# Kernel tuning notes

Hardware: AMD Instinct MI355X
Metric: run time of the kernel (lower is better)

Reference implementation:

```python
import jax, jax.numpy as jnp
import numpy as np
import math

D_MODEL = 512
EXPAND = 2
D_INNER = EXPAND * D_MODEL          # 1024
HEADDIM = 16
NHEADS = D_INNER // HEADDIM         # 64
NGROUPS = 1
D_STATE = 16
D_CONV = 4
CHUNK = 256
CONV_DIM = D_INNER + 2 * NGROUPS * D_STATE      # 1056
D_IN_PROJ = 2 * D_INNER + 2 * NGROUPS * D_STATE + NHEADS  # 2144
EPS = 1e-5


def setup_inputs() -> dict:
    key = jax.random.key(0)
    ks = jax.random.split(key, 9)
    B, L = 2, 4096
    u = jax.random.normal(ks[0], (B, L, D_MODEL), dtype=jnp.float32)
    in_proj_w = jax.random.normal(ks[1], (D_IN_PROJ, D_MODEL), dtype=jnp.float32) * (1.0 / math.sqrt(D_MODEL))
    conv_w = jax.random.normal(ks[2], (CONV_DIM, D_CONV), dtype=jnp.float32) * (1.0 / math.sqrt(D_CONV))
    conv_b = jnp.zeros((CONV_DIM,), dtype=jnp.float32)
    # dt_bias = inverse-softplus of dt sampled log-uniform in [1e-3, 1e-1]
    dt = jnp.exp(jax.random.uniform(ks[3], (NHEADS,)) * (math.log(0.1) - math.log(0.001)) + math.log(0.001))
    dt_bias = dt + jnp.log(-jnp.expm1(-dt))
    A_log = jnp.log(jax.random.uniform(ks[4], (NHEADS,), minval=1.0, maxval=16.0))
    D_skip = jnp.ones((NHEADS,), dtype=jnp.float32)
    norm_w = jnp.ones((D_INNER,), dtype=jnp.float32)
    out_proj_w = jax.random.normal(ks[5], (D_MODEL, D_INNER), dtype=jnp.float32) * (1.0 / math.sqrt(D_INNER))
    return {"u": u, "in_proj_w": in_proj_w, "conv_w": conv_w, "conv_b": conv_b,
            "dt_bias": dt_bias, "A_log": A_log, "D_skip": D_skip,
            "norm_w": norm_w, "out_proj_w": out_proj_w}


def _segsum(x):
    # x: (..., T) -> (..., T, T) lower-triangular cumulative segment sums
    T = x.shape[-1]
    cs = jnp.cumsum(x, axis=-1)
    s = cs[..., :, None] - cs[..., None, :]
    mask = jnp.tril(jnp.ones((T, T), dtype=bool))
    return jnp.where(mask, s, -jnp.inf)


def _ssd(xdt, dA, Bm, Cm):
    # xdt: (b,l,h,p) already multiplied by dt; dA: (b,l,h); Bm,Cm: (b,l,h,n)
    b, l, h, p = xdt.shape
    n = Bm.shape[-1]
    nc = l // CHUNK
    xr = xdt.reshape(b, nc, CHUNK, h, p)
    Br = Bm.reshape(b, nc, CHUNK, h, n)
    Cr = Cm.reshape(b, nc, CHUNK, h, n)
    dAr = dA.reshape(b, nc, CHUNK, h).transpose(0, 3, 1, 2)  # (b,h,nc,c)
    A_cs = jnp.cumsum(dAr, axis=-1)
    # intra-chunk (diagonal blocks)
    Ldec = jnp.exp(_segsum(dAr))                              # (b,h,nc,c,c)
    Y_diag = jnp.einsum('bclhn,bcshn,bhcls,bcshp->bclhp', Cr, Br, Ldec, xr)
    # per-chunk final states
    decay_states = jnp.exp(A_cs[..., -1:] - A_cs)             # (b,h,nc,c)
    states = jnp.einsum('bclhn,bhcl,bclhp->bchpn', Br, decay_states, xr)
    states = jnp.concatenate([jnp.zeros_like(states[:, :1]), states], axis=1)
    chunk_sums = jnp.pad(A_cs[..., -1], ((0, 0), (0, 0), (1, 0)))  # (b,h,nc+1)
    decay_chunk = jnp.exp(_segsum(chunk_sums))                # (b,h,nc+1,nc+1)
    new_states = jnp.einsum('bhzc,bchpn->bzhpn', decay_chunk, states)
    prev_states = new_states[:, :-1]                          # (b,nc,h,p,n)
    # inter-chunk contribution
    state_decay_out = jnp.exp(A_cs)                           # (b,h,nc,c)
    Y_off = jnp.einsum('bclhn,bchpn,bhcl->bclhp', Cr, prev_states, state_decay_out)
    return (Y_diag + Y_off).reshape(b, l, h, p)


def _forward(u, in_proj_w, conv_w, conv_b, dt_bias, A_log, D_skip, norm_w, out_proj_w):
    b, l, _ = u.shape
    zxbcdt = jnp.einsum('bld,ed->ble', u, in_proj_w)
    z = zxbcdt[..., :D_INNER]
    xBC = zxbcdt[..., D_INNER:D_INNER + CONV_DIM]
    dt = zxbcdt[..., D_INNER + CONV_DIM:]
    dt = jax.nn.softplus(dt + dt_bias)                        # (b,l,h)
    # causal depthwise conv1d + silu
    xBC_t = xBC.transpose(0, 2, 1)                            # (b, conv_dim, l)
    conv_out = jax.lax.conv_general_dilated(
        xBC_t, conv_w[:, None, :], window_strides=(1,),
        padding=[(D_CONV - 1, 0)], feature_group_count=CONV_DIM,
        dimension_numbers=('NCH', 'OIH', 'NCH'))
    xBC = jax.nn.silu((conv_out + conv_b[None, :, None]).transpose(0, 2, 1))
    x = xBC[..., :D_INNER].reshape(b, l, NHEADS, HEADDIM)
    Bg = xBC[..., D_INNER:D_INNER + NGROUPS * D_STATE].reshape(b, l, NGROUPS, D_STATE)
    Cg = xBC[..., D_INNER + NGROUPS * D_STATE:].reshape(b, l, NGROUPS, D_STATE)
    hpg = NHEADS // NGROUPS
    Bm = jnp.repeat(Bg, hpg, axis=2)                          # (b,l,h,n)
    Cm = jnp.repeat(Cg, hpg, axis=2)
    A = -jnp.exp(A_log)                                       # (h,)
    dA = dt * A                                               # (b,l,h)
    y = _ssd(x * dt[..., None], dA, Bm, Cm)
    y = y + x * D_skip[None, None, :, None]
    y = y.reshape(b, l, D_INNER)
    # gated RMSNorm (norm_before_gate=False): norm(y * silu(z)) * w
    y = y * jax.nn.silu(z)
    y = y * jax.lax.rsqrt(jnp.mean(y * y, axis=-1, keepdims=True) + EPS) * norm_w
    return jnp.einsum('ble,de->bld', y, out_proj_w)


def reference(u, in_proj_w, conv_w, conv_b, dt_bias, A_log, D_skip, norm_w, out_proj_w):
    return _forward(u, in_proj_w, conv_w, conv_b, dt_bias, A_log, D_skip, norm_w, out_proj_w)
```

## Files before the change

### kernel.cpp

```cpp
#include <hip/hip_runtime.h>
#include <hip/hip_bf16.h>
#include <math.h>

#define D_MODEL   512
#define D_INNER   1024
#define NHEADS    64
#define HEADDIM   16
#define D_STATE   16
#define CONV_DIM  1056
#define D_IN_PROJ 2144
#define CHUNK     256
#define NCHUNK    16
#define BATCH     2
#define SEQ       4096
#define ROWS      (BATCH * SEQ)
#define LDZX      2176
#define TPAD      144

typedef __bf16    bf16x8 __attribute__((ext_vector_type(8)));
typedef _Float16  f16x8  __attribute__((ext_vector_type(8)));
typedef float     f32x4  __attribute__((ext_vector_type(4)));
typedef float     f32x16 __attribute__((ext_vector_type(16)));
typedef unsigned short u16x8 __attribute__((ext_vector_type(8)));
typedef unsigned int   u32x4 __attribute__((ext_vector_type(4)));

__device__ __forceinline__ float softplusf(float x) {
    return (x > 20.f) ? x : log1pf(expf(x));
}
__device__ __forceinline__ float siluf(float x) {
    return x / (1.f + expf(-x));
}
__device__ __forceinline__ unsigned short f2b(float x) {
    union { __hip_bfloat16 h; unsigned short u; } cv;
    cv.h = __float2bfloat16(x);
    return cv.u;
}
__device__ __forceinline__ float b2f(unsigned short u) {
    union { float f; unsigned int i; } c;
    c.i = (unsigned int)u << 16;
    return c.f;
}
__device__ __forceinline__ void load_lds16(const unsigned short* g, unsigned short* l) {
    __builtin_amdgcn_global_load_lds(
        (const __attribute__((address_space(1))) void*)g,
        (__attribute__((address_space(3))) void*)l,
        16, 0, 0);
}

__global__ __launch_bounds__(256) void cast8(const float* __restrict__ in,
                                             unsigned short* __restrict__ out, int n) {
    int i = (blockIdx.x * blockDim.x + threadIdx.x) * 8;
    if (i >= n) return;
    float4 a = *(const float4*)(in + i);
    float4 b = *(const float4*)(in + i + 4);
    u16x8 o;
    o[0] = f2b(a.x); o[1] = f2b(a.y); o[2] = f2b(a.z); o[3] = f2b(a.w);
    o[4] = f2b(b.x); o[5] = f2b(b.y); o[6] = f2b(b.z); o[7] = f2b(b.w);
    *(u16x8*)(out + i) = o;
}

__global__ __launch_bounds__(256) void castpad8(const float* __restrict__ in,
                                                unsigned short* __restrict__ out,
                                                int n, int npad) {
    int i = (blockIdx.x * blockDim.x + threadIdx.x) * 8;
    if (i >= npad) return;
    u16x8 o;
    if (i + 8 <= n) {
        float4 a = *(const float4*)(in + i);
        float4 b = *(const float4*)(in + i + 4);
        o[0] = f2b(a.x); o[1] = f2b(a.y); o[2] = f2b(a.z); o[3] = f2b(a.w);
        o[4] = f2b(b.x); o[5] = f2b(b.y); o[6] = f2b(b.z); o[7] = f2b(b.w);
    } else {
        #pragma unroll
        for (int j = 0; j < 8; ++j) o[j] = (i + j < n) ? f2b(in[i + j]) : (unsigned short)0;
    }
    *(u16x8*)(out + i) = o;
}

__global__ __launch_bounds__(256) void gemm_in(const unsigned short* __restrict__ A,
                                               const unsigned short* __restrict__ B,
                                               unsigned short* __restrict__ C16,
                                               float* __restrict__ dtsp,
                                               const float* __restrict__ dtb) {
    __shared__ unsigned short smem[128 * TPAD];
    const int t    = threadIdx.x;
    const int wave = t >> 6;
    const int lane = t & 63;
    const int bid  = blockIdx.x;
    const int swz  = (bid & 7) * 136 + (bid >> 3);
    const int by   = swz / 17;
    const int bx   = swz - by * 17;
    const int bm   = by * 128;
    const int bn   = bx * 128;
    const int wr   = wave >> 1;
    const int wc   = wave & 1;

    const int srow = wave * 16 + (lane >> 2);
    const int scol = (lane & 3) * 8;
    const unsigned short* ga0 = A + (size_t)(bm + srow) * 512 + scol;
    const unsigned short* ga1 = A + (size_t)(bm + 64 + srow) * 512 + scol;
    const unsigned short* gb0 = B + (size_t)(bn + srow) * 512 + scol;
    const unsigned short* gb1 = B + (size_t)(bn + 64 + srow) * 512 + scol;

    const int fr = lane & 15;
    const int kb = (lane >> 4) * 8;

    f32x4 acc[4][4] = {};

    load_lds16(ga0, smem + wave * 512);
    load_lds16(ga1, smem + 2048 + wave * 512);
    load_lds16(gb0, smem + 8192 + wave * 512);
    load_lds16(gb1, smem + 8192 + 2048 + wave * 512);
    __syncthreads();

    int cur = 0;
    for (int it = 0; it < 16; ++it) {
        if (it + 1 < 16) {
            const int k0 = (it + 1) * 32;
            const int nb = cur ^ 1;
            load_lds16(ga0 + k0, smem + nb * 4096 + wave * 512);
            load_lds16(ga1 + k0, smem + nb * 4096 + 2048 + wave * 512);
            load_lds16(gb0 + k0, smem + 8192 + nb * 4096 + wave * 512);
            load_lds16(gb1 + k0, smem + 8192 + nb * 4096 + 2048 + wave * 512);
        }
        const unsigned short* Ab = smem + cur * 4096;
        const unsigned short* Bb = smem + 8192 + cur * 4096;
        bf16x8 af[4], bfr[4];
        #pragma unroll
        for (int m = 0; m < 4; ++m)
            af[m] = *reinterpret_cast<const bf16x8*>(&Ab[(wr * 64 + m * 16 + fr) * 32 + kb]);
        #pragma unroll
        for (int n = 0; n < 4; ++n)
            bfr[n] = *reinterpret_cast<const bf16x8*>(&Bb[(wc * 64 + n * 16 + fr) * 32 + kb]);
        #pragma unroll
        for (int m = 0; m < 4; ++m)
            #pragma unroll
            for (int n = 0; n < 4; ++n)
                acc[m][n] = __builtin_amdgcn_mfma_f32_16x16x32_bf16(af[m], bfr[n], acc[m][n], 0, 0, 0);
        __syncthreads();
        cur ^= 1;
    }

    if (bn == 2048) {
        #pragma unroll
        for (int m = 0; m < 4; ++m) {
            #pragma unroll
            for (int n = 0; n < 4; ++n) {
                const int col = bn + wc * 64 + fr + n * 16;
                if (col >= 2080 && col < 2144) {
                    const int h = col - 2080;
                    const float bias = dtb[h];
                    #pragma unroll
                    for (int j = 0; j < 4; ++j) {
                        const int row = bm + wr * 64 + ((lane >> 4) << 2) + m * 16 + j;
                        dtsp[(size_t)row * 64 + h] = softplusf(acc[m][n][j] + bias);
                    }
                }
            }
        }
    }
    #pragma unroll
    for (int m = 0; m < 4; ++m) {
        #pragma unroll
        for (int n = 0; n < 4; ++n) {
            const int lcol = wc * 64 + fr + n * 16;
            #pragma unroll
            for (int j = 0; j < 4; ++j) {
                const int lrow = wr * 64 + ((lane >> 4) << 2) + m * 16 + j;
                smem[lrow * TPAD + lcol] = f2b(acc[m][n][j]);
            }
        }
    }
    __syncthreads();
    #pragma unroll
    for (int p = 0; p < 8; ++p) {
        const int r = p * 16 + (t >> 4);
        const int cl = (t & 15) * 8;
        u16x8 v = *(const u16x8*)&smem[r * TPAD + cl];
        *(u16x8*)(C16 + (size_t)(bm + r) * LDZX + bn + cl) = v;
    }
}

__global__ __launch_bounds__(256) void gemm_out(const unsigned short* __restrict__ A,
                                                const unsigned short* __restrict__ B,
                                                float* __restrict__ C) {
    __shared__ unsigned short smem[12288];
    const int t    = threadIdx.x;
    const int wave = t >> 6;
    const int lane = t & 63;
    const int bm   = blockIdx.y * 128;
    const int bn   = blockIdx.x * 64;
    const int wr   = wave >> 1;
    const int wc   = wave & 1;

    const int srow = wave * 16 + (lane >> 2);
    const int scol = (lane & 3) * 8;
    const unsigned short* ga0 = A + (size_t)(bm + srow) * 1024 + scol;
    const unsigned short* ga1 = A + (size_t)(bm + 64 + srow) * 1024 + scol;
    const unsigned short* gb0 = B + (size_t)(bn + srow) * 1024 + scol;

    const int fr = lane & 15;
    const int kb = (lane >> 4) * 8;

    f32x4 acc[4][2] = {};

    load_lds16(ga0, smem + wave * 512);
    load_lds16(ga1, smem + 2048 + wave * 512);
    load_lds16(gb0, smem + 8192 + wave * 512);
    __syncthreads();

    int cur = 0;
    for (int it = 0; it < 32; ++it) {
        if (it + 1 < 32) {
            const int k0 = (it + 1) * 32;
            const int nb = cur ^ 1;
            load_lds16(ga0 + k0, smem + nb * 4096 + wave * 512);
            load_lds16(ga1 + k0, smem + nb * 4096 + 2048 + wave * 512);
            load_lds16(gb0 + k0, smem + 8192 + nb * 2048 + wave * 512);
        }
        const unsigned short* Ab = smem + cur * 4096;
        const unsigned short* Bb = smem + 8192 + cur * 2048;
        bf16x8 af[4], bfr[2];
        #pragma unroll
        for (int m = 0; m < 4; ++m)
            af[m] = *reinterpret_cast<const bf16x8*>(&Ab[(wr * 64 + m * 16 + fr) * 32 + kb]);
        #pragma unroll
        for (int n = 0; n < 2; ++n)
            bfr[n] = *reinterpret_cast<const bf16x8*>(&Bb[(wc * 32 + n * 16 + fr) * 32 + kb]);
        #pragma unroll
        for (int m = 0; m < 4; ++m)
            #pragma unroll
            for (int n = 0; n < 2; ++n)
                acc[m][n] = __builtin_amdgcn_mfma_f32_16x16x32_bf16(af[m], bfr[n], acc[m][n], 0, 0, 0);
        __syncthreads();
        cur ^= 1;
    }

    const int cr0 = bm + wr * 64 + ((lane >> 4) << 2);
    const int cc0 = bn + wc * 32 + fr;
    #pragma unroll
    for (int m = 0; m < 4; ++m)
        #pragma unroll
        for (int n = 0; n < 2; ++n)
            #pragma unroll
            for (int j = 0; j < 4; ++j)
                C[(size_t)(cr0 + m * 16 + j) * 512 + cc0 + n * 16] = acc[m][n][j];
}

__global__ void conv_silu44(const unsigned short* __restrict__ zxb, const float* __restrict__ cw,
                            const float* __restrict__ cb, unsigned short* __restrict__ xcb) {
    int idx = blockIdx.x * blockDim.x + threadIdx.x;
    if (idx >= (ROWS / 4) * (CONV_DIM / 4)) return;
    const int cq  = idx % (CONV_DIM / 4);
    const int blq = idx / (CONV_DIM / 4);
    const int bl0 = blq * 4;
    const int l0  = bl0 % SEQ;
    const int c4  = cq * 4;
    const unsigned short* base = zxb + (size_t)bl0 * LDZX + D_INNER + c4;
    float4 w0 = *(const float4*)(cw + (c4 + 0) * 4);
    float4 w1 = *(const float4*)(cw + (c4 + 1) * 4);
    float4 w2 = *(const float4*)(cw + (c4 + 2) * 4);
    float4 w3 = *(const float4*)(cw + (c4 + 3) * 4);
    float4 bb = *(const float4*)(cb + c4);
    float4 in[7];
    #pragma unroll
    for (int k = 0; k < 7; ++k) {
        const int off = k - 3;
        if (l0 == 0 && k < 3) {
            in[k] = make_float4(0.f, 0.f, 0.f, 0.f);
        } else {
            ushort4 uu = *(const ushort4*)(base + (long)off * LDZX);
            in[k] = make_float4(b2f(uu.x), b2f(uu.y), b2f(uu.z), b2f(uu.w));
        }
    }
    #pragma unroll
    for (int r = 0; r < 4; ++r) {
        ushort4 o;
        o.x = f2b(siluf(bb.x + w0.x * in[r].x + w0.y * in[r + 1].x + w0.z * in[r + 2].x + w0.w * in[r + 3].x));
        o.y = f2b(siluf(bb.y + w1.x * in[r].y + w1.y * in[r + 1].y + w1.z * in[r + 2].y + w1.w * in[r + 3].y));
        o.z = f2b(siluf(bb.z + w2.x * in[r].z + w2.y * in[r + 1].z + w2.z * in[r + 2].z + w2.w * in[r + 3].z));
        o.w = f2b(siluf(bb.w + w3.x * in[r].w + w3.y * in[r + 1].w + w3.z * in[r + 2].w + w3.w * in[r + 3].w));
        *(ushort4*)(xcb + (size_t)(bl0 + r) * CONV_DIM + c4) = o;
    }
}

__global__ __launch_bounds__(256, 3) void ssd_chunk(const unsigned short* __restrict__ xcb,
                                                    const float* __restrict__ dtsp,
                                                    const float* __restrict__ A_log,
                                                    unsigned short* __restrict__ ypre16,
                                                    float* __restrict__ states,
                                                    float* __restrict__ csb,
                                                    float* __restrict__ csum) {
    __shared__ _Float16 Bb[256][16];
    __shared__ _Float16 Cb[256][16];
    __shared__ _Float16 Xt[16][264];
    __shared__ _Float16 Xdt[16][264];
    __shared__ _Float16 Bt[16][264];
    __shared__ float csL[256];
    __shared__ float wsumL[4];
    __shared__ float stpart[4][16][16];

    const int bid = blockIdx.x;
    const int h = bid & 63;
    const int c = (bid >> 6) & 15;
    const int b = bid >> 10;
    const int t = threadIdx.x;
    const int wv = t >> 6;
    const int lane = t & 63;
    const int fr = lane & 15;
    const int hi = lane >> 4;
    const int l31 = lane & 31;
    const int hi5 = lane >> 5;
    const int row = b * SEQ + c * CHUNK + t;

    float Ah  = -__expf(A_log[h]);
    float dtv = dtsp[(size_t)row * NHEADS + h];
    float val = dtv * Ah;
    #pragma unroll
    for (int off = 1; off < 64; off <<= 1) {
        float o = __shfl_up(val, off, 64);
        if (lane >= off) val += o;
    }
    if (lane == 63) wsumL[wv] = val;
    __syncthreads();
    float pre = 0.f, cl = 0.f;
    #pragma unroll
    for (int w2 = 0; w2 < 4; ++w2) {
        float s = wsumL[w2];
        if (w2 < wv) pre += s;
        cl += s;
    }
    float cst = val + pre;
    csL[t] = cst;
    csb[(size_t)bid * 256 + t] = cst;
    if (t == 0) csum[(b * 64 + h) * 16 + c] = cl;
    float dec_t = __expf(cl - cst);

    const unsigned short* xrow = xcb + (size_t)row * CONV_DIM;
    u16x8 braw0 = *(const u16x8*)(xrow + D_INNER);
    u16x8 braw1 = *(const u16x8*)(xrow + D_INNER + 8);
    u16x8 craw0 = *(const u16x8*)(xrow + D_INNER + D_STATE);
    u16x8 craw1 = *(const u16x8*)(xrow + D_INNER + D_STATE + 8);
    u16x8 xraw0 = *(const u16x8*)(xrow + h * HEADDIM);
    u16x8 xraw1 = *(const u16x8*)(xrow + h * HEADDIM + 8);
    float bv[16], cv[16], xv[16];
    #pragma unroll
    for (int n = 0; n < 8; ++n) {
        bv[n] = b2f(braw0[n]); bv[8 + n] = b2f(braw1[n]);
        cv[n] = b2f(craw0[n]); cv[8 + n] = b2f(craw1[n]);
        xv[n] = b2f(xraw0[n]); xv[8 + n] = b2f(xraw1[n]);
    }
    {
        f16x8 pk;
        #pragma unroll
        for (int n = 0; n < 8; ++n) pk[n] = (_Float16)cv[n];
        *(f16x8*)&Cb[t][0] = pk;
        #pragma unroll
        for (int n = 0; n < 8; ++n) pk[n] = (_Float16)cv[8 + n];
        *(f16x8*)&Cb[t][8] = pk;
        #pragma unroll
        for (int n = 0; n < 8; ++n) pk[n] = (_Float16)bv[n];
        *(f16x8*)&Bb[t][0] = pk;
        #pragma unroll
        for (int n = 0; n < 8; ++n) pk[n] = (_Float16)bv[8 + n];
        *(f16x8*)&Bb[t][8] = pk;
    }
    #pragma unroll
    for (int n = 0; n < 16; ++n) {
        Bt[n][t] = (_Float16)bv[n];
        float xd = xv[n] * dtv;
        Xt[n][t] = (_Float16)xd;
        Xdt[n][t] = (_Float16)(xd * dec_t);
    }
    __syncthreads();

    const int browbase = b * SEQ + c * CHUNK;
    const f32x16 z16 = {};

    #pragma unroll
    for (int halfi = 0; halfi < 2; ++halfi) {
        const int rt = (halfi == 0) ? wv : 7 - wv;
        const int t0 = rt * 32;
        const float cs_t = csL[t0 + l31];
        const f16x8 cfrag = *(const f16x8*)&Cb[t0 + l31][hi5 * 8];
        f32x16 yacc = {};
        for (int sb = 0; sb <= rt; ++sb) {
            const int s0 = sb * 32;
            f16x8 bfrag = *(const f16x8*)&Bb[s0 + l31][hi5 * 8];
            f32x16 sp = __builtin_amdgcn_mfma_f32_32x32x16_f16(bfrag, cfrag, z16, 0, 0, 0);
            const bool diag = (sb == rt);
            unsigned int D[8];
            #pragma unroll
            for (int j = 0; j < 8; ++j) {
                const int q0 = 2 * j;
                const int sr0 = (q0 & 3) + 8 * (q0 >> 2) + 4 * hi5;
                float p0 = sp[q0] * __expf(cs_t - csL[s0 + sr0]);
                float p1 = sp[q0 + 1] * __expf(cs_t - csL[s0 + sr0 + 1]);
                if (diag) {
                    p0 = (sr0 <= l31) ? p0 : 0.f;
                    p1 = (sr0 + 1 <= l31) ? p1 : 0.f;
                }
                D[j] = __builtin_bit_cast(unsigned int, __builtin_amdgcn_cvt_pkrtz(p0, p1));
            }
            unsigned int pD[8];
            #pragma unroll
            for (int j = 0; j < 8; ++j) pD[j] = (unsigned int)__shfl_xor((int)D[j], 32, 64);
            u32x4 fa;
            fa[0] = hi5 ? pD[2] : D[0];
            fa[1] = hi5 ? pD[3] : D[1];
            fa[2] = hi5 ? D[2] : pD[0];
            fa[3] = hi5 ? D[3] : pD[1];
            f16x8 pf0 = __builtin_bit_cast(f16x8, fa);
            f16x8 xf0 = *(const f16x8*)&Xt[fr][s0 + hi5 * 8];
            yacc = __builtin_amdgcn_mfma_f32_32x32x16_f16(pf0, xf0, yacc, 0, 0, 0);
            fa[0] = hi5 ? pD[6] : D[4];
            fa[1] = hi5 ? pD[7] : D[5];
            fa[2] = hi5 ? D[6] : pD[4];
            fa[3] = hi5 ? D[7] : pD[5];
            f16x8 pf1 = __builtin_bit_cast(f16x8, fa);
            f16x8 xf1 = *(const f16x8*)&Xt[fr][s0 + 16 + hi5 * 8];
            yacc = __builtin_amdgcn_mfma_f32_32x32x16_f16(pf1, xf1, yacc, 0, 0, 0);
        }
        if (l31 < 16) {
            #pragma unroll
            for (int q = 0; q < 16; ++q) {
                const int tr = t0 + (q & 3) + 8 * (q >> 2) + 4 * hi5;
                ypre16[(size_t)(browbase + tr) * D_INNER + h * HEADDIM + l31] = f2b(yacc[q]);
            }
        }
    }

    const int r0w = wv * 64;
    f32x4 stacc = {};
    #pragma unroll
    for (int kt = 0; kt < 2; ++kt) {
        f16x8 xa = *(const f16x8*)&Xdt[fr][r0w + kt * 32 + hi * 8];
        f16x8 bb2 = *(const f16x8*)&Bt[fr][r0w + kt * 32 + hi * 8];
        stacc = __builtin_amdgcn_mfma_f32_16x16x32_f16(xa, bb2, stacc, 0, 0, 0);
    }
    #pragma unroll
    for (int j = 0; j < 4; ++j)
        stpart[wv][hi * 4 + j][fr] = stacc[j];
    __syncthreads();
    {
        const int p = t >> 4, n = t & 15;
        float st = stpart[0][p][n] + stpart[1][p][n] + stpart[2][p][n] + stpart[3][p][n];
        states[(size_t)bid * 256 + t] = st;
    }
}

__global__ __launch_bounds__(256) void ssd_rec(const float* __restrict__ states,
                                               const float* __restrict__ csum,
                                               float* __restrict__ prevst) {
    __shared__ float dec[16];
    const int bh = blockIdx.x;
    const int b = bh >> 6, h = bh & 63;
    const int t = threadIdx.x;
    if (t < 16) dec[t] = __expf(csum[bh * 16 + t]);
    float sv[16];
    #pragma unroll
    for (int c = 0; c < NCHUNK; ++c)
        sv[c] = states[((size_t)((b * 16 + c) * 64 + h)) * 256 + t];
    __syncthreads();
    float run = 0.f;
    #pragma unroll
    for (int c = 0; c < NCHUNK; ++c) {
        prevst[((size_t)((b * 16 + c) * 64 + h)) * 256 + t] = run;
        run = run * dec[c] + sv[c];
    }
}

__global__ __launch_bounds__(512, 4) void ssd_off_norm(const unsigned short* __restrict__ xcb,
                                                       const unsigned short* __restrict__ zxb,
                                                       const unsigned short* __restrict__ ypre16,
                                                       const float* __restrict__ prevst,
                                                       const float* __restrict__ csb,
                                                       const float* __restrict__ Dskip,
                                                       const float* __restrict__ normw,
                                                       unsigned short* __restrict__ yout) {
    __shared__ float Cs[16][16];
    __shared__ float csS[64][16];
    __shared__ float nw[1024];
    __shared__ float Dn[64];
    __shared__ float red[16][8];

    const int blk = blockIdx.x;
    const int bc = blk >> 4;
    const int rb = blk & 15;
    const int r0 = rb * 16;
    const int b = bc >> 4, c = bc & 15;
    const int brow0 = b * SEQ + c * CHUNK;
    const int t = threadIdx.x;
    const int ch0 = t * 2;
    const int h = ch0 >> 4;
    const int p0 = ch0 & 15;
    const int wv = t >> 6;
    const int lane = t & 63;

    if (t < 256) *(float4*)&nw[t * 4] = *(const float4*)(normw + t * 4);
    else if (t < 320) Dn[t - 256] = Dskip[t - 256];
    if (t < 64) {
        int r = t >> 2, n4 = (t & 3) * 4;
        ushort4 uu = *(const ushort4*)(xcb + (size_t)(brow0 + r0 + r) * CONV_DIM
                                       + D_INNER + D_STATE + n4);
        Cs[r][n4 + 0] = b2f(uu.x); Cs[r][n4 + 1] = b2f(uu.y);
        Cs[r][n4 + 2] = b2f(uu.z); Cs[r][n4 + 3] = b2f(uu.w);
    }
    #pragma unroll
    for (int i = t; i < 1024; i += 512) {
        int r = i & 15, hh = i >> 4;
        csS[hh][r] = csb[(size_t)(bc * 64 + hh) * 256 + r0 + r];
    }

    float ps[2][16];
    {
        const float* pbase = prevst + (size_t)(bc * 64 + h) * 256 + p0 * 16;
        #pragma unroll
        for (int n4 = 0; n4 < 16; n4 += 4) {
            *(float4*)&ps[0][n4] = *(const float4*)(pbase + n4);
            *(float4*)&ps[1][n4] = *(const float4*)(pbase + 16 + n4);
        }
    }
    __syncthreads();

    const float d = Dn[h];
    const float nw0 = nw[ch0], nw1 = nw[ch0 + 1];

    for (int r = 0; r < 16; ++r) {
        const size_t grow = (size_t)(brow0 + r0 + r);
        ushort2 yu = *(const ushort2*)(ypre16 + grow * D_INNER + ch0);
        ushort2 xu = *(const ushort2*)(xcb + grow * CONV_DIM + ch0);
        ushort2 zu = *(const ushort2*)(zxb + grow * LDZX + ch0);
        float sdo = __expf(csS[h][r]);
        float off0 = 0.f, off1 = 0.f;
        #pragma unroll
        for (int n = 0; n < 16; ++n) {
            float cn = Cs[r][n];
            off0 += cn * ps[0][n];
            off1 += cn * ps[1][n];
        }
        float g0 = (b2f(yu.x) + sdo * off0 + b2f(xu.x) * d) * siluf(b2f(zu.x));
        float g1 = (b2f(yu.y) + sdo * off1 + b2f(xu.y) * d) * siluf(b2f(zu.y));
        float s = g0 * g0 + g1 * g1;
        #pragma unroll
        for (int o = 32; o > 0; o >>= 1) s += __shfl_down(s, o, 64);
        if (lane == 0) red[r][wv] = s;
        __syncthreads();
        float tot = 0.f;
        #pragma unroll
        for (int w2 = 0; w2 < 8; ++w2) tot += red[r][w2];
        float rstd = rsqrtf(tot * (1.f / (float)D_INNER) + 1e-5f);
        ushort2 o2;
        o2.x = f2b(g0 * rstd * nw0);
        o2.y = f2b(g1 * rstd * nw1);
        *(ushort2*)(yout + grow * D_INNER + ch0) = o2;
    }
}

extern "C" void kernel_launch(void* const* d_in, const int* in_sizes, int n_in,
                              void* d_out, int out_size, void* d_ws, size_t ws_size,
                              hipStream_t stream) {
    const float* u     = (const float*)d_in[0];
    const float* Win   = (const float*)d_in[1];
    const float* cw    = (const float*)d_in[2];
    const float* cb    = (const float*)d_in[3];
    const float* dtb   = (const float*)d_in[4];
    const float* Alog  = (const float*)d_in[5];
    const float* Dsk   = (const float*)d_in[6];
    const float* normw = (const float*)d_in[7];
    const float* Wout  = (const float*)d_in[8];
    float* out = (float*)d_out;

    float* ws = (float*)d_ws;
    unsigned short* zxb = (unsigned short*)ws;
    float* dtsp   = ws + 8912896;
    float* csb    = dtsp + 524288;
    float* st     = csb + 524288;
    float* pst    = st + 524288;
    float* csum   = pst + 524288;
    unsigned short* ypre16 = (unsigned short*)(csum + 2048);
    unsigned short* xcb    = (unsigned short*)((float*)ypre16 + 4194304);
    unsigned short* yn_bf  = (unsigned short*)((float*)xcb + 4325376);
    unsigned short* u_bf   = (unsigned short*)((float*)yn_bf + 2097152);
    unsigned short* win_bf  = (unsigned short*)((float*)u_bf + 2097152);
    unsigned short* wout_bf = (unsigned short*)((float*)win_bf + 557056);

    cast8<<<2048, 256, 0, stream>>>(u, u_bf, 4194304);
    castpad8<<<544, 256, 0, stream>>>(Win, win_bf, 2144 * 512, 2176 * 512);
    cast8<<<256, 256, 0, stream>>>(Wout, wout_bf, 524288);

    gemm_in<<<1088, 256, 0, stream>>>(u_bf, win_bf, zxb, dtsp, dtb);

    conv_silu44<<<(ROWS / 4) * (CONV_DIM / 4) / 256, 256, 0, stream>>>(zxb, cw, cb, xcb);
    ssd_chunk<<<BATCH * NCHUNK * NHEADS, 256, 0, stream>>>(xcb, dtsp, Alog, ypre16, st, csb, csum);
    ssd_rec<<<BATCH * NHEADS, 256, 0, stream>>>(st, csum, pst);
    ssd_off_norm<<<512, 512, 0, stream>>>(xcb, zxb, ypre16, pst, csb, Dsk, normw, yn_bf);

    gemm_out<<<dim3(8, 64), 256, 0, stream>>>(yn_bf, wout_bf, out);
}
```

Baseline: 148.6 us.

## Merge cast kernels, shrink SSD chunk LDS, batch norm reductions under one barrier

The three fp32-to-bf16 cast launches become one kernel that branches on block index, removing two launches. In ssd_chunk the decay-scaled X buffer is replaced by a per-row fp16 decay vector applied at MFMA load time, and the state partials reuse the Cb buffer. The smaller LDS footprint lets the launch bound move to 4 blocks per SM. The norm kernel computes all 16 rows first, then does a single barrier instead of one per row. The gemm_in output staging drops its padded stride to a plain 128 stride, which may add LDS bank conflicts. The decay multiply is now done in fp16, which slightly changes precision.

```diff
diff --git a/kernel.cpp b/kernel.cpp
--- a/kernel.cpp
+++ b/kernel.cpp
@@ -15,7 +15,6 @@
 #define SEQ       4096
 #define ROWS      (BATCH * SEQ)
 #define LDZX      2176
-#define TPAD      144
 
 typedef __bf16    bf16x8 __attribute__((ext_vector_type(8)));
 typedef _Float16  f16x8  __attribute__((ext_vector_type(8)));
@@ -47,34 +46,42 @@
         16, 0, 0);
 }
 
-__global__ __launch_bounds__(256) void cast8(const float* __restrict__ in,
-                                             unsigned short* __restrict__ out, int n) {
-    int i = (blockIdx.x * blockDim.x + threadIdx.x) * 8;
-    if (i >= n) return;
-    float4 a = *(const float4*)(in + i);
-    float4 b = *(const float4*)(in + i + 4);
+__global__ __launch_bounds__(256) void cast_all(const float* __restrict__ u,
+                                                const float* __restrict__ Win,
+                                                const float* __restrict__ Wout,
+                                                unsigned short* __restrict__ u_bf,
+                                                unsigned short* __restrict__ win_bf,
+                                                unsigned short* __restrict__ wout_bf) {
+    const int bid = blockIdx.x;
     u16x8 o;
-    o[0] = f2b(a.x); o[1] = f2b(a.y); o[2] = f2b(a.z); o[3] = f2b(a.w);
-    o[4] = f2b(b.x); o[5] = f2b(b.y); o[6] = f2b(b.z); o[7] = f2b(b.w);
-    *(u16x8*)(out + i) = o;
-}
-
-__global__ __launch_bounds__(256) void castpad8(const float* __restrict__ in,
-                                                unsigned short* __restrict__ out,
-                                                int n, int npad) {
-    int i = (blockIdx.x * blockDim.x + threadIdx.x) * 8;
-    if (i >= npad) return;
-    u16x8 o;
-    if (i + 8 <= n) {
-        float4 a = *(const float4*)(in + i);
-        float4 b = *(const float4*)(in + i + 4);
+    if (bid < 2048) {
+        const int i = (bid * 256 + threadIdx.x) * 8;
+        float4 a = *(const float4*)(u + i);
+        float4 b = *(const float4*)(u + i + 4);
         o[0] = f2b(a.x); o[1] = f2b(a.y); o[2] = f2b(a.z); o[3] = f2b(a.w);
         o[4] = f2b(b.x); o[5] = f2b(b.y); o[6] = f2b(b.z); o[7] = f2b(b.w);
+        *(u16x8*)(u_bf + i) = o;
+    } else if (bid < 2592) {
+        const int i = ((bid - 2048) * 256 + threadIdx.x) * 8;
+        const int n = 2144 * 512;
+        if (i + 8 <= n) {
+            float4 a = *(const float4*)(Win + i);
+            float4 b = *(const float4*)(Win + i + 4);
+            o[0] = f2b(a.x); o[1] = f2b(a.y); o[2] = f2b(a.z); o[3] = f2b(a.w);
+            o[4] = f2b(b.x); o[5] = f2b(b.y); o[6] = f2b(b.z); o[7] = f2b(b.w);
+        } else {
+            #pragma unroll
+            for (int j = 0; j < 8; ++j) o[j] = (i + j < n) ? f2b(Win[i + j]) : (unsigned short)0;
+        }
+        *(u16x8*)(win_bf + i) = o;
     } else {
-        #pragma unroll
-        for (int j = 0; j < 8; ++j) o[j] = (i + j < n) ? f2b(in[i + j]) : (unsigned short)0;
-    }
-    *(u16x8*)(out + i) = o;
+        const int i = ((bid - 2592) * 256 + threadIdx.x) * 8;
+        float4 a = *(const float4*)(Wout + i);
+        float4 b = *(const float4*)(Wout + i + 4);
+        o[0] = f2b(a.x); o[1] = f2b(a.y); o[2] = f2b(a.z); o[3] = f2b(a.w);
+        o[4] = f2b(b.x); o[5] = f2b(b.y); o[6] = f2b(b.z); o[7] = f2b(b.w);
+        *(u16x8*)(wout_bf + i) = o;
+    }
 }
 
 __global__ __launch_bounds__(256) void gemm_in(const unsigned short* __restrict__ A,
@@ -82,7 +89,7 @@
                                                unsigned short* __restrict__ C16,
                                                float* __restrict__ dtsp,
                                                const float* __restrict__ dtb) {
-    __shared__ unsigned short smem[128 * TPAD];
+    __shared__ unsigned short smem[16384];
     const int t    = threadIdx.x;
     const int wave = t >> 6;
     const int lane = t & 63;
@@ -167,7 +174,7 @@
             #pragma unroll
             for (int j = 0; j < 4; ++j) {
                 const int lrow = wr * 64 + ((lane >> 4) << 2) + m * 16 + j;
-                smem[lrow * TPAD + lcol] = f2b(acc[m][n][j]);
+                smem[lrow * 128 + lcol] = f2b(acc[m][n][j]);
             }
         }
     }
@@ -176,7 +183,7 @@
     for (int p = 0; p < 8; ++p) {
         const int r = p * 16 + (t >> 4);
         const int cl = (t & 15) * 8;
-        u16x8 v = *(const u16x8*)&smem[r * TPAD + cl];
+        u16x8 v = *(const u16x8*)&smem[r * 128 + cl];
         *(u16x8*)(C16 + (size_t)(bm + r) * LDZX + bn + cl) = v;
     }
 }
@@ -284,7 +291,7 @@
     }
 }
 
-__global__ __launch_bounds__(256, 3) void ssd_chunk(const unsigned short* __restrict__ xcb,
+__global__ __launch_bounds__(256, 4) void ssd_chunk(const unsigned short* __restrict__ xcb,
                                                     const float* __restrict__ dtsp,
                                                     const float* __restrict__ A_log,
                                                     unsigned short* __restrict__ ypre16,
@@ -294,11 +301,10 @@
     __shared__ _Float16 Bb[256][16];
     __shared__ _Float16 Cb[256][16];
     __shared__ _Float16 Xt[16][264];
-    __shared__ _Float16 Xdt[16][264];
     __shared__ _Float16 Bt[16][264];
     __shared__ float csL[256];
+    __shared__ __align__(16) _Float16 decL[256];
     __shared__ float wsumL[4];
-    __shared__ float stpart[4][16][16];
 
     const int bid = blockIdx.x;
     const int h = bid & 63;
@@ -334,7 +340,7 @@
     csL[t] = cst;
     csb[(size_t)bid * 256 + t] = cst;
     if (t == 0) csum[(b * 64 + h) * 16 + c] = cl;
-    float dec_t = __expf(cl - cst);
+    decL[t] = (_Float16)__expf(cl - cst);
 
     const unsigned short* xrow = xcb + (size_t)row * CONV_DIM;
     u16x8 braw0 = *(const u16x8*)(xrow + D_INNER);
@@ -368,9 +374,7 @@
     #pragma unroll
     for (int n = 0; n < 16; ++n) {
         Bt[n][t] = (_Float16)bv[n];
-        float xd = xv[n] * dtv;
-        Xt[n][t] = (_Float16)xd;
-        Xdt[n][t] = (_Float16)(xd * dec_t);
+        Xt[n][t] = (_Float16)(xv[n] * dtv);
     }
     __syncthreads();
 
@@ -430,21 +434,27 @@
         }
     }
 
+    __syncthreads();
+    float* stpart = (float*)&Cb[0][0];
     const int r0w = wv * 64;
     f32x4 stacc = {};
     #pragma unroll
     for (int kt = 0; kt < 2; ++kt) {
-        f16x8 xa = *(const f16x8*)&Xdt[fr][r0w + kt * 32 + hi * 8];
-        f16x8 bb2 = *(const f16x8*)&Bt[fr][r0w + kt * 32 + hi * 8];
+        const int sbase = r0w + kt * 32 + hi * 8;
+        f16x8 xa = *(const f16x8*)&Xt[fr][sbase];
+        f16x8 dd = *(const f16x8*)&decL[sbase];
+        xa = xa * dd;
+        f16x8 bb2 = *(const f16x8*)&Bt[fr][sbase];
         stacc = __builtin_amdgcn_mfma_f32_16x16x32_f16(xa, bb2, stacc, 0, 0, 0);
     }
     #pragma unroll
     for (int j = 0; j < 4; ++j)
-        stpart[wv][hi * 4 + j][fr] = stacc[j];
+        stpart[wv * 256 + (hi * 4 + j) * 16 + fr] = stacc[j];
     __syncthreads();
     {
         const int p = t >> 4, n = t & 15;
-        float st = stpart[0][p][n] + stpart[1][p][n] + stpart[2][p][n] + stpart[3][p][n];
+        float st = stpart[0 * 256 + p * 16 + n] + stpart[1 * 256 + p * 16 + n]
+                 + stpart[2 * 256 + p * 16 + n] + stpart[3 * 256 + p * 16 + n];
         states[(size_t)bid * 256 + t] = st;
     }
 }
@@ -526,6 +536,8 @@
     const float d = Dn[h];
     const float nw0 = nw[ch0], nw1 = nw[ch0 + 1];
 
+    float g0r[16], g1r[16];
+    #pragma unroll
     for (int r = 0; r < 16; ++r) {
         const size_t grow = (size_t)(brow0 + r0 + r);
         ushort2 yu = *(const ushort2*)(ypre16 + grow * D_INNER + ch0);
@@ -541,18 +553,23 @@
         }
         float g0 = (b2f(yu.x) + sdo * off0 + b2f(xu.x) * d) * siluf(b2f(zu.x));
         float g1 = (b2f(yu.y) + sdo * off1 + b2f(xu.y) * d) * siluf(b2f(zu.y));
+        g0r[r] = g0; g1r[r] = g1;
         float s = g0 * g0 + g1 * g1;
         #pragma unroll
         for (int o = 32; o > 0; o >>= 1) s += __shfl_down(s, o, 64);
         if (lane == 0) red[r][wv] = s;
-        __syncthreads();
+    }
+    __syncthreads();
+    #pragma unroll
+    for (int r = 0; r < 16; ++r) {
+        const size_t grow = (size_t)(brow0 + r0 + r);
         float tot = 0.f;
         #pragma unroll
         for (int w2 = 0; w2 < 8; ++w2) tot += red[r][w2];
         float rstd = rsqrtf(tot * (1.f / (float)D_INNER) + 1e-5f);
         ushort2 o2;
-        o2.x = f2b(g0 * rstd * nw0);
-        o2.y = f2b(g1 * rstd * nw1);
+        o2.x = f2b(g0r[r] * rstd * nw0);
+        o2.y = f2b(g1r[r] * rstd * nw1);
         *(ushort2*)(yout + grow * D_INNER + ch0) = o2;
     }
 }
@@ -585,9 +602,7 @@
     unsigned short* win_bf  = (unsigned short*)((float*)u_bf + 2097152);
     unsigned short* wout_bf = (unsigned short*)((float*)win_bf + 557056);
 
-    cast8<<<2048, 256, 0, stream>>>(u, u_bf, 4194304);
-    castpad8<<<544, 256, 0, stream>>>(Win, win_bf, 2144 * 512, 2176 * 512);
-    cast8<<<256, 256, 0, stream>>>(Wout, wout_bf, 524288);
+    cast_all<<<2848, 256, 0, stream>>>(u, Win, Wout, u_bf, win_bf, wout_bf);
 
     gemm_in<<<1088, 256, 0, stream>>>(u_bf, win_bf, zxb, dtsp, dtb);
 
```

After: 143.2 us. 3.6% less time.
